# Kernel tuning notes

Measured on AMD Instinct MI355X. Metric: run time of the kernel, lower is better.

The kernel has to match this reference:

```python
import jax, jax.numpy as jnp
import numpy as np

B, T, D, H = 1, 2049, 1024, 16
HD = D // H                      # head_dim = 64
MAX_SEQ = 1025
L = 2 * MAX_SEQ - 1              # = T (required by the module's relative shift)

def setup_inputs() -> dict:
    key = jax.random.key(0)
    ks = jax.random.split(key, 12)
    s = 0.02
    return {
        'q': jax.random.normal(ks[0], (B, T, D), dtype=jnp.float32),
        'k': jax.random.normal(ks[1], (B, T, D), dtype=jnp.float32),
        'v': jax.random.normal(ks[2], (B, T, D), dtype=jnp.float32),
        'mask': jnp.tril(jnp.ones((1, 1, T, T), dtype=jnp.int32)),  # causal
        'Wq_w': jax.random.normal(ks[3], (D, D), dtype=jnp.float32) * s,
        'Wq_b': jnp.zeros((D,), dtype=jnp.float32),
        'Wk_w': jax.random.normal(ks[4], (D, D), dtype=jnp.float32) * s,
        'Wk_b': jnp.zeros((D,), dtype=jnp.float32),
        'Wv_w': jax.random.normal(ks[5], (D, D), dtype=jnp.float32) * s,
        'Wv_b': jnp.zeros((D,), dtype=jnp.float32),
        'Er': jax.random.normal(ks[6], (L, HD), dtype=jnp.float32),
        'Wo_w': jax.random.normal(ks[7], (D, D), dtype=jnp.float32) * s,
        'Wo_b': jnp.zeros((D,), dtype=jnp.float32),
    }

def reference(q, k, v, mask, Wq_w, Wq_b, Wk_w, Wk_b, Wv_w, Wv_b, Er, Wo_w, Wo_b):
    b, t, d = q.shape
    def proj(x, w, bias):
        # nn.Linear: x @ W^T + b ; then (B,T,H,HD) -> (B,H,T,HD)
        return (x @ w.T + bias).reshape(b, t, H, HD).transpose(0, 2, 1, 3)
    qh = proj(q, Wq_w, Wq_b)
    kh = proj(k, Wk_w, Wk_b)
    vh = proj(v, Wv_w, Wv_b)
    scores = jnp.einsum('bhtd,bhsd->bhts', qh, kh)          # (B,H,T,T)
    QEr = jnp.einsum('bhtd,ld->bhtl', qh, Er)               # (B,H,T,L) with L == T
    # _relative_shift: pad a zero row on seq dim then drop first row ->
    # row i becomes QEr row i+1, last row zeros (faithful to torch code)
    rel = jnp.concatenate([QEr[:, :, 1:, :], jnp.zeros_like(QEr[:, :, :1, :])], axis=2)
    scores = scores + rel
    scores = jnp.where(mask[:, :, :t, :t] == 0, -jnp.inf, scores)
    attn = jax.nn.softmax(scores / (HD ** 0.5), axis=-1)
    ctx = jnp.einsum('bhts,bhsd->bthd', attn, vh).reshape(b, t, d)
    return ctx @ Wo_w.T + Wo_b
```

## Files before the change

kernel.cpp:

```cpp
#include <hip/hip_runtime.h>
#include <hip/hip_bf16.h>
#include <math.h>

constexpr int T_SEQ = 2049;
constexpr int D_MODEL = 1024;
constexpr int N_HEAD = 16;
constexpr int HEAD_DIM = 64;
constexpr int VT_STRIDE = 2112;
constexpr int T1_ROWS = 1152;

typedef __attribute__((ext_vector_type(8))) short short8;
typedef __attribute__((ext_vector_type(4))) short short4v;
typedef __attribute__((ext_vector_type(4))) float floatx4;

__device__ inline void load_lds16(const void* g, void* l) {
  __builtin_amdgcn_global_load_lds(
      (const __attribute__((address_space(1))) unsigned int*)g,
      (__attribute__((address_space(3))) unsigned int*)l, 16, 0, 0);
}

__device__ inline short8 cvt8_bf16(const float* p) {
  float4 a = *(const float4*)p, b = *(const float4*)(p + 4);
  __hip_bfloat16 t[8] = {__float2bfloat16(a.x), __float2bfloat16(a.y),
                         __float2bfloat16(a.z), __float2bfloat16(a.w),
                         __float2bfloat16(b.x), __float2bfloat16(b.y),
                         __float2bfloat16(b.z), __float2bfloat16(b.w)};
  return *(const short8*)t;
}

__device__ inline float bf2f(__hip_bfloat16 x) { return __bfloat162float(x); }

__global__ __launch_bounds__(256) void cast_all(
    const float* __restrict__ q, const float* __restrict__ k,
    const float* __restrict__ v, const float* __restrict__ wq,
    const float* __restrict__ wk, const float* __restrict__ wv,
    const float* __restrict__ er, __hip_bfloat16* __restrict__ qo,
    __hip_bfloat16* __restrict__ ko, __hip_bfloat16* __restrict__ vo,
    __hip_bfloat16* __restrict__ wqo, __hip_bfloat16* __restrict__ wko,
    __hip_bfloat16* __restrict__ wvo, __hip_bfloat16* __restrict__ ero) {
  const int z = blockIdx.y;
  const float* in;
  __hip_bfloat16* out;
  int n;
  switch (z) {
    case 0: in = q; out = qo; n = T_SEQ * D_MODEL; break;
    case 1: in = k; out = ko; n = T_SEQ * D_MODEL; break;
    case 2: in = v; out = vo; n = T_SEQ * D_MODEL; break;
    case 3: in = wq; out = wqo; n = D_MODEL * D_MODEL; break;
    case 4: in = wk; out = wko; n = D_MODEL * D_MODEL; break;
    case 5: in = wv; out = wvo; n = D_MODEL * D_MODEL; break;
    default: in = er; out = ero; n = T_SEQ * HEAD_DIM; break;
  }
  const int i = (blockIdx.x * 256 + threadIdx.x) * 8;
  if (i + 8 > n) return;
  *(short8*)(out + i) = cvt8_bf16(in + i);
}

template <int BN, int OUTK>
__global__ __launch_bounds__(256) void mfma_gemm(
    const __hip_bfloat16* __restrict__ A0, const __hip_bfloat16* __restrict__ A1,
    const __hip_bfloat16* __restrict__ A2, const __hip_bfloat16* __restrict__ W0,
    const __hip_bfloat16* __restrict__ W1, const __hip_bfloat16* __restrict__ W2,
    const float* __restrict__ bias0, const float* __restrict__ bias1,
    const float* __restrict__ bias2, void* C0, void* C1, void* C2, int M) {
  constexpr int K = D_MODEL;
  constexpr int BK = 32;
  constexpr int NT = BN / 32;
  constexpr int AINST = 2;
  constexpr int BINST = BN / 64;
  constexpr int NLOADS = AINST + BINST;
  __shared__ __align__(16) char smem[128 * 64 * 2 + BN * 64 * 2];
  __hip_bfloat16* As = (__hip_bfloat16*)smem;
  __hip_bfloat16* Bs = (__hip_bfloat16*)(smem + 128 * 64 * 2);

  const int z = blockIdx.z;
  const short* A = (const short*)(z == 0 ? A0 : z == 1 ? A1 : A2);
  const short* W = (const short*)(z == 0 ? W0 : z == 1 ? W1 : W2);
  const float* bias = z == 0 ? bias0 : z == 1 ? bias1 : bias2;
  void* C = z == 0 ? C0 : z == 1 ? C1 : C2;

  const int tid = threadIdx.x;
  const int wave = tid >> 6, lane = tid & 63;
  const int col = lane & 15, quad = lane >> 4;
  const int wm = wave >> 1, wn = wave & 1;
  const int m0 = blockIdx.y * 128, n0 = blockIdx.x * BN;

  const int srow = lane >> 2;
  const int sslot = lane & 3;

  floatx4 acc[4][NT];
#pragma unroll
  for (int i = 0; i < 4; i++)
#pragma unroll
    for (int j = 0; j < NT; j++) acc[i][j] = (floatx4){0.f, 0.f, 0.f, 0.f};

#define STAGE_G(K0, BUF)                                                      \
  {                                                                           \
    _Pragma("unroll") for (int i = 0; i < AINST; i++) {                       \
      const int r_ = (wave * AINST + i) * 16 + srow;                          \
      const int ch = sslot ^ ((r_ >> 1) & 3);                                 \
      const int am = min(m0 + r_, M - 1);                                     \
      load_lds16(A + (size_t)am * K + (K0) + ch * 8,                          \
                 (char*)As + (BUF)*8192 + (wave * AINST + i) * 1024);         \
    }                                                                         \
    _Pragma("unroll") for (int i = 0; i < BINST; i++) {                       \
      const int r_ = (wave * BINST + i) * 16 + srow;                          \
      const int ch = sslot ^ ((r_ >> 1) & 3);                                 \
      load_lds16(W + (size_t)(n0 + r_) * K + (K0) + ch * 8,                   \
                 (char*)Bs + (BUF) * (BN * 64) + (wave * BINST + i) * 1024);  \
    }                                                                         \
  }

  STAGE_G(0, 0)

  int buf = 0;
  for (int k0 = 0; k0 < K; k0 += BK, buf ^= 1) {
    if (k0 + BK < K) {
      STAGE_G(k0 + BK, buf ^ 1)
      asm volatile("s_waitcnt vmcnt(%0)" ::"i"(NLOADS) : "memory");
    } else {
      asm volatile("s_waitcnt vmcnt(0)" ::: "memory");
    }
    __builtin_amdgcn_s_barrier();

    const __hip_bfloat16* as = As + buf * 4096;
    const __hip_bfloat16* bs = Bs + buf * (BN * 32);
    short8 af[4], bfr[NT];
#pragma unroll
    for (int t = 0; t < 4; t++) {
      const int ra = wm * 64 + t * 16 + col;
      af[t] = *(const short8*)(as + ra * 32 + ((quad ^ ((ra >> 1) & 3)) * 8));
    }
#pragma unroll
    for (int t = 0; t < NT; t++) {
      const int rb = wn * (BN / 2) + t * 16 + col;
      bfr[t] = *(const short8*)(bs + rb * 32 + ((quad ^ ((rb >> 1) & 3)) * 8));
    }
#pragma unroll
    for (int mt = 0; mt < 4; mt++)
#pragma unroll
      for (int nt = 0; nt < NT; nt++)
        acc[mt][nt] = __builtin_amdgcn_mfma_f32_16x16x32_bf16(af[mt], bfr[nt],
                                                              acc[mt][nt], 0, 0, 0);
    asm volatile("" ::: "memory");
    __builtin_amdgcn_s_barrier();
  }
#undef STAGE_G

  if (OUTK == 2 && z == 2) {
    short* Tt = (short*)smem;
#pragma unroll
    for (int mt = 0; mt < 4; mt++) {
      const int mb = wm * 16 + mt * 4 + quad;
#pragma unroll
      for (int nt = 0; nt < NT; nt++) {
        const int n = wn * (BN / 2) + nt * 16 + col;
        const float bb = bias[n0 + n];
        __hip_bfloat16 pk[4];
#pragma unroll
        for (int r = 0; r < 4; r++) pk[r] = __float2bfloat16(acc[mt][nt][r] + bb);
        *(short4v*)((char*)Tt + n * 256 + ((mb ^ (n & 15)) << 3)) =
            *(const short4v*)pk;
      }
    }
    __syncthreads();
    const int n_loc = tid >> 1, half = tid & 1;
    if (m0 + half * 64 < VT_STRIDE) {
      const int ng = n0 + n_loc;
      __hip_bfloat16* dst = (__hip_bfloat16*)C +
                            ((size_t)(ng >> 6) * HEAD_DIM + (ng & 63)) * VT_STRIDE +
                            m0 + half * 64;
#pragma unroll
      for (int c = 0; c < 8; c++) {
        short4v lo = *(const short4v*)((char*)Tt + n_loc * 256 +
                                       (((half * 16 + 2 * c) ^ (n_loc & 15)) << 3));
        short4v hi = *(const short4v*)((char*)Tt + n_loc * 256 +
                                       (((half * 16 + 2 * c + 1) ^ (n_loc & 15)) << 3));
        short8 o8 = {lo[0], lo[1], lo[2], lo[3], hi[0], hi[1], hi[2], hi[3]};
        *(short8*)((short*)dst + c * 8) = o8;
      }
    }
    return;
  }

#pragma unroll
  for (int mt = 0; mt < 4; mt++) {
#pragma unroll
    for (int r = 0; r < 4; r++) {
      const int m = m0 + wm * 64 + mt * 16 + quad * 4 + r;
      if (m >= M) continue;
#pragma unroll
      for (int nt = 0; nt < NT; nt++) {
        const int n = n0 + wn * (BN / 2) + nt * 16 + col;
        const float val = acc[mt][nt][r] + bias[n];
        if (OUTK == 0) {
          ((float*)C)[(size_t)m * D_MODEL + n] = val;
        } else {
          const int h = n >> 6, hd = n & 63;
          ((__hip_bfloat16*)C)[((size_t)h * T_SEQ + m) * HEAD_DIM + hd] =
              __float2bfloat16(val);
        }
      }
    }
  }
}

__global__ __launch_bounds__(512, 4) void flash_attn(
    const __hip_bfloat16* __restrict__ qh, const __hip_bfloat16* __restrict__ kh,
    const __hip_bfloat16* __restrict__ er, const __hip_bfloat16* __restrict__ vt,
    __hip_bfloat16* __restrict__ ctx, __hip_bfloat16* __restrict__ O0,
    __hip_bfloat16* __restrict__ O1, float* __restrict__ l0g,
    float* __restrict__ l1g) {
  __shared__ __align__(16) __hip_bfloat16 Ks[2][64 * 128];
  __shared__ __align__(16) __hip_bfloat16 Vs[2][64 * 64];
  __shared__ __align__(16) __hip_bfloat16 Ps[8][1024];

  const int tid = threadIdx.x;
  const int id = blockIdx.x + 26 * blockIdx.y;
  const int slot = id >> 3;
  const int h = (id & 7) + 8 * (slot >= 26);
  const int b = 25 - (slot >= 26 ? slot - 26 : slot);

  const int qt = (b < 8) ? b : 8 + ((b - 8) >> 1);
  const int tq0 = qt * 128;
  const int jmax = min(tq0 + 127, T_SEQ - 1) >> 6;
  int j0, j1;
  bool alt;
  if (b < 8) {
    j0 = 0; j1 = jmax; alt = false;
  } else {
    const int mid = (jmax + 1) >> 1;
    alt = (b - 8) & 1;
    j0 = alt ? mid : 0;
    j1 = alt ? jmax : mid - 1;
  }

  const int wave = tid >> 6;
  const int lane = tid & 63;
  const int col = lane & 15;
  const int quad = lane >> 4;

  const short* qplane = (const short*)(qh + (size_t)h * T_SEQ * HEAD_DIM);
  const short* kplane = (const short*)(kh + (size_t)h * T_SEQ * HEAD_DIM);
  const short* eplane = (const short*)er;
  const short* vplane = (const short*)(vt + (size_t)h * HEAD_DIM * VT_STRIDE);

  const int t_abs = tq0 + wave * 16 + col;
  const int tload = min(t_abs, T_SEQ - 1);
  const bool hiz = (t_abs >= T_SEQ - 1);
  short8 aq[4];
#pragma unroll
  for (int kc = 0; kc < 4; kc++) {
    short8 v = *(const short8*)(qplane + (size_t)tload * 64 + kc * 32 + quad * 8);
    if (kc >= 2 && hiz) v = (short8){0, 0, 0, 0, 0, 0, 0, 0};
    aq[kc] = v;
  }

  floatx4 o[4];
  float l_lane = 0.f;
#pragma unroll
  for (int i = 0; i < 4; i++) o[i] = (floatx4){0.f, 0.f, 0.f, 0.f};

  const int tstrip = tq0 + wave * 16;
  __hip_bfloat16* psw = &Ps[wave][0];

#define STAGE_TILE(JJ, BUF)                                                        \
  {                                                                                \
    const int s0_ = (JJ) * 64;                                                     \
    _Pragma("unroll") for (int ii = 0; ii < 2; ii++) {                             \
      const int i_ = wave * 2 + ii;                                                \
      const int r_ = i_ * 4 + (lane >> 4);                                         \
      const int sl_ = lane & 15;                                                   \
      const int g_ = (sl_ & 8) | ((sl_ ^ (r_ & 7)) & 7);                           \
      const int s_ = min(s0_ + r_, T_SEQ - 1);                                     \
      const short* src_ = (g_ < 8) ? (kplane + (size_t)s_ * 64 + g_ * 8)           \
                                   : (eplane + (size_t)s_ * 64 + (g_ - 8) * 8);    \
      load_lds16(src_, (char*)&Ks[BUF][0] + i_ * 1024);                            \
    }                                                                              \
    {                                                                              \
      const int d_ = wave * 8 + (lane >> 3);                                       \
      const int sl_ = lane & 7;                                                    \
      const int g_ = sl_ ^ (d_ & 7);                                               \
      load_lds16(vplane + (size_t)d_ * VT_STRIDE + s0_ + g_ * 8,                   \
                 (char*)&Vs[BUF][0] + wave * 1024);                                \
    }                                                                              \
  }

  STAGE_TILE(j0, 0)
  int buf = 0;

  for (int j = j0; j <= j1; ++j, buf ^= 1) {
    __syncthreads();
    if (j < j1) STAGE_TILE(j + 1, buf ^ 1)

    const int s0 = j * 64;
    if (s0 > tstrip + 15) continue;

    const __hip_bfloat16* ks = &Ks[buf][0];
    const __hip_bfloat16* vs = &Vs[buf][0];

    floatx4 sacc[4];
    __builtin_amdgcn_s_setprio(1);
#pragma unroll
    for (int st = 0; st < 4; st++) {
      floatx4 c = {0.f, 0.f, 0.f, 0.f};
      const int row = st * 16 + col;
#pragma unroll
      for (int kc = 0; kc < 4; kc++) {
        const int ch = kc * 4 + quad;
        const int slot2 = (ch & 8) | ((ch ^ (row & 7)) & 7);
        short8 ka = *(const short8*)(ks + row * 128 + slot2 * 8);
        c = __builtin_amdgcn_mfma_f32_16x16x32_bf16(ka, aq[kc], c, 0, 0, 0);
      }
      sacc[st] = c;
    }
    __builtin_amdgcn_s_setprio(0);

    if (s0 + 63 > tstrip) {
#pragma unroll
      for (int st = 0; st < 4; st++) {
        const int sbase = s0 + st * 16 + quad * 4;
#pragma unroll
        for (int r = 0; r < 4; r++)
          if (sbase + r > t_abs) sacc[st][r] = -INFINITY;
      }
    }

    float rs = 0.f;
#pragma unroll
    for (int st = 0; st < 4; st++)
#pragma unroll
      for (int r = 0; r < 4; r++) {
        const float p = __expf(sacc[st][r] * 0.125f);
        sacc[st][r] = p;
        rs += p;
      }
    l_lane += rs;

#pragma unroll
    for (int st = 0; st < 4; st++) {
      __hip_bfloat16 pb[4];
#pragma unroll
      for (int r = 0; r < 4; r++) pb[r] = __float2bfloat16(sacc[st][r]);
      const int kcA = st >> 1;
      const int quadA = (st & 1) * 2 + (quad >> 1);
      const int off = ((kcA * 4 + quadA) * 16 + col) * 8 + (quad & 1) * 4;
      *(short4v*)(psw + off) = *(const short4v*)pb;
    }
    short8 pa[2];
#pragma unroll
    for (int kc = 0; kc < 2; kc++)
      pa[kc] = *(const short8*)(psw + ((kc * 4 + quad) * 16 + col) * 8);

    __builtin_amdgcn_s_setprio(1);
#pragma unroll
    for (int nt = 0; nt < 4; nt++) {
      const int row = nt * 16 + col;
#pragma unroll
      for (int kc = 0; kc < 2; kc++) {
        const int slot2 = (kc * 4 + quad) ^ (row & 7);
        short8 vb = *(const short8*)(vs + row * 64 + slot2 * 8);
        o[nt] = __builtin_amdgcn_mfma_f32_16x16x32_bf16(pa[kc], vb, o[nt], 0, 0, 0);
      }
    }
    __builtin_amdgcn_s_setprio(0);
  }

  l_lane += __shfl_xor(l_lane, 16, 64);
  l_lane += __shfl_xor(l_lane, 32, 64);

  if (b < 8) {
    const float linv = 1.0f / l_lane;
    float linv_r[4];
#pragma unroll
    for (int r = 0; r < 4; r++) linv_r[r] = __shfl(linv, quad * 4 + r, 64);
#pragma unroll
    for (int r = 0; r < 4; r++) {
      const int t = tstrip + quad * 4 + r;
#pragma unroll
      for (int nt = 0; nt < 4; nt++)
        ctx[(size_t)t * D_MODEL + h * 64 + nt * 16 + col] =
            __float2bfloat16(o[nt][r] * linv_r[r]);
    }
  } else {
    if (lane < 16) {
      const int t = tstrip + lane;
      if (t < T_SEQ) {
        if (!alt)
          l0g[h * T1_ROWS + (t - 1024)] = l_lane;
        else
          l1g[h * T1_ROWS + (t - 1024)] = l_lane;
      }
    }
#pragma unroll
    for (int r = 0; r < 4; r++) {
      const int t = tstrip + quad * 4 + r;
      if (t < T_SEQ) {
        __hip_bfloat16* dst = (!alt ? O0 : O1) + (size_t)(t - 1024) * D_MODEL;
#pragma unroll
        for (int nt = 0; nt < 4; nt++)
          dst[h * 64 + nt * 16 + col] = __float2bfloat16(o[nt][r]);
      }
    }
  }
}

__global__ __launch_bounds__(256) void finalize(
    const __hip_bfloat16* __restrict__ O0, const __hip_bfloat16* __restrict__ O1,
    const float* __restrict__ l0g, const float* __restrict__ l1g,
    __hip_bfloat16* __restrict__ ctx, const float* __restrict__ wo_src,
    __hip_bfloat16* __restrict__ wob) {
  if (blockIdx.y == 1) {
    const int i = (blockIdx.x * 256 + threadIdx.x) * 8;
    if (i + 8 <= D_MODEL * D_MODEL) *(short8*)(wob + i) = cvt8_bf16(wo_src + i);
    return;
  }
  const int idx = blockIdx.x * 256 + threadIdx.x;
  const int tr = idx >> 7;
  const int t = 1024 + tr;
  if (t >= T_SEQ) return;
  const int ch = idx & 127;
  const int h = ch >> 3;

  const float l = l0g[h * T1_ROWS + tr] + l1g[h * T1_ROWS + tr];
  const __hip_bfloat16* a = O0 + (size_t)tr * D_MODEL + ch * 8;
  const __hip_bfloat16* bsrc = O1 + (size_t)tr * D_MODEL + ch * 8;
  const float inv = 1.0f / l;
  __hip_bfloat16 outv[8];
#pragma unroll
  for (int i = 0; i < 8; i++)
    outv[i] = __float2bfloat16((bf2f(a[i]) + bf2f(bsrc[i])) * inv);
  *(short8*)(ctx + (size_t)t * D_MODEL + ch * 8) = *(const short8*)outv;
}

extern "C" void kernel_launch(void* const* d_in, const int* in_sizes, int n_in,
                              void* d_out, int out_size, void* d_ws, size_t ws_size,
                              hipStream_t stream) {
  const float* q = (const float*)d_in[0];
  const float* k = (const float*)d_in[1];
  const float* v = (const float*)d_in[2];
  const float* Wq_w = (const float*)d_in[4];
  const float* Wq_b = (const float*)d_in[5];
  const float* Wk_w = (const float*)d_in[6];
  const float* Wk_b = (const float*)d_in[7];
  const float* Wv_w = (const float*)d_in[8];
  const float* Wv_b = (const float*)d_in[9];
  const float* Er = (const float*)d_in[10];
  const float* Wo_w = (const float*)d_in[11];
  const float* Wo_b = (const float*)d_in[12];
  float* out = (float*)d_out;

  char* ws = (char*)d_ws;
  const size_t sz_plane = (size_t)T_SEQ * D_MODEL * 2;
  const size_t sz_w = (size_t)D_MODEL * D_MODEL * 2;
  const size_t sz_vt = (size_t)N_HEAD * HEAD_DIM * VT_STRIDE * 2;
  const size_t sz_er = (size_t)T_SEQ * HEAD_DIM * 2;
  const size_t sz_Op = (size_t)T1_ROWS * D_MODEL * 2;
  const size_t sz_l = (size_t)N_HEAD * T1_ROWS * 4;

  __hip_bfloat16* qbf = (__hip_bfloat16*)ws;
  __hip_bfloat16* kbf = (__hip_bfloat16*)(ws + sz_plane);
  __hip_bfloat16* vbf = (__hip_bfloat16*)(ws + 2 * sz_plane);
  __hip_bfloat16* wqb = (__hip_bfloat16*)(ws + 3 * sz_plane);
  __hip_bfloat16* wkb = (__hip_bfloat16*)(ws + 3 * sz_plane + sz_w);
  __hip_bfloat16* wvb = (__hip_bfloat16*)(ws + 3 * sz_plane + 2 * sz_w);
  char* hi = ws + 3 * sz_plane + 3 * sz_w;
  __hip_bfloat16* qpr = (__hip_bfloat16*)hi;
  __hip_bfloat16* kpr = (__hip_bfloat16*)(hi + sz_plane);
  __hip_bfloat16* vt = (__hip_bfloat16*)(hi + 2 * sz_plane);
  __hip_bfloat16* er_bf = (__hip_bfloat16*)(hi + 2 * sz_plane + sz_vt);

  __hip_bfloat16* ctxb = (__hip_bfloat16*)ws;
  __hip_bfloat16* O0 = (__hip_bfloat16*)(ws + sz_plane);
  __hip_bfloat16* O1 = (__hip_bfloat16*)(ws + sz_plane + sz_Op);
  float* l0g = (float*)(ws + sz_plane + 2 * sz_Op);
  float* l1g = (float*)(ws + sz_plane + 2 * sz_Op + sz_l);
  __hip_bfloat16* wob = (__hip_bfloat16*)(ws + 3 * sz_plane);

  const dim3 blk(256);

  cast_all<<<dim3(1025, 7), blk, 0, stream>>>(q, k, v, Wq_w, Wk_w, Wv_w, Er, qbf,
                                              kbf, vbf, wqb, wkb, wvb, er_bf);

  mfma_gemm<128, 2><<<dim3(8, 17, 3), blk, 0, stream>>>(
      qbf, kbf, vbf, wqb, wkb, wvb, Wq_b, Wk_b, Wv_b, qpr, kpr, vt, T_SEQ);

  flash_attn<<<dim3(26, N_HEAD), dim3(512), 0, stream>>>(qpr, kpr, er_bf, vt, ctxb,
                                                         O0, O1, l0g, l1g);

  finalize<<<dim3((1025 * 128 + 255) / 256, 2), blk, 0, stream>>>(
      O0, O1, l0g, l1g, ctxb, Wo_w, wob);

  mfma_gemm<64, 0><<<dim3(16, 17, 1), blk, 0, stream>>>(
      ctxb, ctxb, ctxb, wob, wob, wob, Wo_b, Wo_b, Wo_b, out, out, out, T_SEQ);
}
```

Before: 192.6 us.

## Fuse fp32-to-bf16 casts into GEMM loaders and merge split-attention finalize into output GEMM

Removes the standalone cast kernel and the finalize kernel. The QKV GEMM now reads fp32 activations and weights directly, converts them to bf16 in registers and writes them into LDS through a software-pipelined register prefetch, and the Er cast rides along as an extra z-slice. The output GEMM merges the two partial attention outputs with their softmax normalizers inside its A-loader and converts Wo on the fly. This cuts two launches and the bf16 intermediate write/read traffic, but the GEMMs now load twice the bytes per element and lose the async global-to-LDS loads, and each weight tile is reconverted by every M-block.

New measurement: 208.3 us. 8.2% more time.

```diff
diff --git a/kernel.cpp b/kernel.cpp
--- a/kernel.cpp
+++ b/kernel.cpp
@@ -28,133 +28,133 @@
   return *(const short8*)t;
 }
 
+__device__ inline short8 cvt8_pair(float4 a, float4 b) {
+  __hip_bfloat16 t[8] = {__float2bfloat16(a.x), __float2bfloat16(a.y),
+                         __float2bfloat16(a.z), __float2bfloat16(a.w),
+                         __float2bfloat16(b.x), __float2bfloat16(b.y),
+                         __float2bfloat16(b.z), __float2bfloat16(b.w)};
+  return *(const short8*)t;
+}
+
 __device__ inline float bf2f(__hip_bfloat16 x) { return __bfloat162float(x); }
 
-__global__ __launch_bounds__(256) void cast_all(
+__global__ __launch_bounds__(256) void qkv_gemm(
     const float* __restrict__ q, const float* __restrict__ k,
     const float* __restrict__ v, const float* __restrict__ wq,
     const float* __restrict__ wk, const float* __restrict__ wv,
-    const float* __restrict__ er, __hip_bfloat16* __restrict__ qo,
-    __hip_bfloat16* __restrict__ ko, __hip_bfloat16* __restrict__ vo,
-    __hip_bfloat16* __restrict__ wqo, __hip_bfloat16* __restrict__ wko,
-    __hip_bfloat16* __restrict__ wvo, __hip_bfloat16* __restrict__ ero) {
-  const int z = blockIdx.y;
-  const float* in;
-  __hip_bfloat16* out;
-  int n;
-  switch (z) {
-    case 0: in = q; out = qo; n = T_SEQ * D_MODEL; break;
-    case 1: in = k; out = ko; n = T_SEQ * D_MODEL; break;
-    case 2: in = v; out = vo; n = T_SEQ * D_MODEL; break;
-    case 3: in = wq; out = wqo; n = D_MODEL * D_MODEL; break;
-    case 4: in = wk; out = wko; n = D_MODEL * D_MODEL; break;
-    case 5: in = wv; out = wvo; n = D_MODEL * D_MODEL; break;
-    default: in = er; out = ero; n = T_SEQ * HEAD_DIM; break;
-  }
-  const int i = (blockIdx.x * 256 + threadIdx.x) * 8;
-  if (i + 8 > n) return;
-  *(short8*)(out + i) = cvt8_bf16(in + i);
-}
-
-template <int BN, int OUTK>
-__global__ __launch_bounds__(256) void mfma_gemm(
-    const __hip_bfloat16* __restrict__ A0, const __hip_bfloat16* __restrict__ A1,
-    const __hip_bfloat16* __restrict__ A2, const __hip_bfloat16* __restrict__ W0,
-    const __hip_bfloat16* __restrict__ W1, const __hip_bfloat16* __restrict__ W2,
-    const float* __restrict__ bias0, const float* __restrict__ bias1,
-    const float* __restrict__ bias2, void* C0, void* C1, void* C2, int M) {
-  constexpr int K = D_MODEL;
-  constexpr int BK = 32;
-  constexpr int NT = BN / 32;
-  constexpr int AINST = 2;
-  constexpr int BINST = BN / 64;
-  constexpr int NLOADS = AINST + BINST;
-  __shared__ __align__(16) char smem[128 * 64 * 2 + BN * 64 * 2];
-  __hip_bfloat16* As = (__hip_bfloat16*)smem;
-  __hip_bfloat16* Bs = (__hip_bfloat16*)(smem + 128 * 64 * 2);
-
+    const float* __restrict__ bq, const float* __restrict__ bk,
+    const float* __restrict__ bv, __hip_bfloat16* __restrict__ qpr,
+    __hip_bfloat16* __restrict__ kpr, __hip_bfloat16* __restrict__ vt,
+    const float* __restrict__ er, __hip_bfloat16* __restrict__ er_bf) {
   const int z = blockIdx.z;
-  const short* A = (const short*)(z == 0 ? A0 : z == 1 ? A1 : A2);
-  const short* W = (const short*)(z == 0 ? W0 : z == 1 ? W1 : W2);
-  const float* bias = z == 0 ? bias0 : z == 1 ? bias1 : bias2;
-  void* C = z == 0 ? C0 : z == 1 ? C1 : C2;
+  if (z == 3) {
+    const int id = blockIdx.x + 8 * blockIdx.y;
+    const int i = (id * 256 + threadIdx.x) * 8;
+    if (i + 8 <= T_SEQ * HEAD_DIM) *(short8*)(er_bf + i) = cvt8_bf16(er + i);
+    return;
+  }
+  constexpr int K = D_MODEL, BK = 32, NS = K / BK;
+  __shared__ __align__(16) char smem[32768];
+
+  const float* A = z == 0 ? q : z == 1 ? k : v;
+  const float* W = z == 0 ? wq : z == 1 ? wk : wv;
+  const float* bias = z == 0 ? bq : z == 1 ? bk : bv;
 
   const int tid = threadIdx.x;
   const int wave = tid >> 6, lane = tid & 63;
   const int col = lane & 15, quad = lane >> 4;
   const int wm = wave >> 1, wn = wave & 1;
-  const int m0 = blockIdx.y * 128, n0 = blockIdx.x * BN;
-
-  const int srow = lane >> 2;
-  const int sslot = lane & 3;
-
-  floatx4 acc[4][NT];
+  const int m0 = blockIdx.y * 128, n0 = blockIdx.x * 128;
+  const int srow = lane >> 2, sslot = lane & 3;
+
+  int rrow[2], rch[2], ram[2];
+#pragma unroll
+  for (int i = 0; i < 2; i++) {
+    rrow[i] = (wave * 2 + i) * 16 + srow;
+    rch[i] = sslot ^ ((rrow[i] >> 1) & 3);
+    ram[i] = min(m0 + rrow[i], T_SEQ - 1);
+  }
+
+  float4 ra[2][2], rb[2][2];
+  short8 SA[2], SB[2];
+
+#define LOADS(K0)                                                          \
+  {                                                                        \
+    _Pragma("unroll") for (int i = 0; i < 2; i++) {                        \
+      const float* p = A + (size_t)ram[i] * K + (K0) + rch[i] * 8;         \
+      ra[i][0] = *(const float4*)p;                                        \
+      ra[i][1] = *(const float4*)(p + 4);                                  \
+      const float* pw = W + (size_t)(n0 + rrow[i]) * K + (K0) + rch[i] * 8;\
+      rb[i][0] = *(const float4*)pw;                                       \
+      rb[i][1] = *(const float4*)(pw + 4);                                 \
+    }                                                                      \
+  }
+#define CVT()                                                              \
+  {                                                                        \
+    _Pragma("unroll") for (int i = 0; i < 2; i++) {                        \
+      SA[i] = cvt8_pair(ra[i][0], ra[i][1]);                               \
+      SB[i] = cvt8_pair(rb[i][0], rb[i][1]);                               \
+    }                                                                      \
+  }
+
+  floatx4 acc[4][4];
 #pragma unroll
   for (int i = 0; i < 4; i++)
 #pragma unroll
-    for (int j = 0; j < NT; j++) acc[i][j] = (floatx4){0.f, 0.f, 0.f, 0.f};
-
-#define STAGE_G(K0, BUF)                                                      \
-  {                                                                           \
-    _Pragma("unroll") for (int i = 0; i < AINST; i++) {                       \
-      const int r_ = (wave * AINST + i) * 16 + srow;                          \
-      const int ch = sslot ^ ((r_ >> 1) & 3);                                 \
-      const int am = min(m0 + r_, M - 1);                                     \
-      load_lds16(A + (size_t)am * K + (K0) + ch * 8,                          \
-                 (char*)As + (BUF)*8192 + (wave * AINST + i) * 1024);         \
-    }                                                                         \
-    _Pragma("unroll") for (int i = 0; i < BINST; i++) {                       \
-      const int r_ = (wave * BINST + i) * 16 + srow;                          \
-      const int ch = sslot ^ ((r_ >> 1) & 3);                                 \
-      load_lds16(W + (size_t)(n0 + r_) * K + (K0) + ch * 8,                   \
-                 (char*)Bs + (BUF) * (BN * 64) + (wave * BINST + i) * 1024);  \
-    }                                                                         \
-  }
-
-  STAGE_G(0, 0)
-
-  int buf = 0;
-  for (int k0 = 0; k0 < K; k0 += BK, buf ^= 1) {
-    if (k0 + BK < K) {
-      STAGE_G(k0 + BK, buf ^ 1)
-      asm volatile("s_waitcnt vmcnt(%0)" ::"i"(NLOADS) : "memory");
-    } else {
-      asm volatile("s_waitcnt vmcnt(0)" ::: "memory");
-    }
+    for (int j = 0; j < 4; j++) acc[i][j] = (floatx4){0.f, 0.f, 0.f, 0.f};
+
+  LOADS(0)
+  CVT()
+  LOADS(BK)
+
+  for (int s = 0; s < NS; ++s) {
+    const int buf = s & 1;
+#pragma unroll
+    for (int i = 0; i < 2; i++) {
+      *(short8*)(smem + buf * 8192 + rrow[i] * 64 + sslot * 16) = SA[i];
+      *(short8*)(smem + 16384 + buf * 8192 + rrow[i] * 64 + sslot * 16) = SB[i];
+    }
+    asm volatile("s_waitcnt lgkmcnt(0)" ::: "memory");
+    __builtin_amdgcn_sched_barrier(0);
     __builtin_amdgcn_s_barrier();
 
-    const __hip_bfloat16* as = As + buf * 4096;
-    const __hip_bfloat16* bs = Bs + buf * (BN * 32);
-    short8 af[4], bfr[NT];
+    const __hip_bfloat16* as = (const __hip_bfloat16*)(smem + buf * 8192);
+    const __hip_bfloat16* bs = (const __hip_bfloat16*)(smem + 16384 + buf * 8192);
+    short8 af[4], bfr[4];
 #pragma unroll
     for (int t = 0; t < 4; t++) {
-      const int ra = wm * 64 + t * 16 + col;
-      af[t] = *(const short8*)(as + ra * 32 + ((quad ^ ((ra >> 1) & 3)) * 8));
-    }
-#pragma unroll
-    for (int t = 0; t < NT; t++) {
-      const int rb = wn * (BN / 2) + t * 16 + col;
-      bfr[t] = *(const short8*)(bs + rb * 32 + ((quad ^ ((rb >> 1) & 3)) * 8));
+      const int ra_ = wm * 64 + t * 16 + col;
+      af[t] = *(const short8*)(as + ra_ * 32 + ((quad ^ ((ra_ >> 1) & 3)) * 8));
+    }
+#pragma unroll
+    for (int t = 0; t < 4; t++) {
+      const int rb_ = wn * 64 + t * 16 + col;
+      bfr[t] = *(const short8*)(bs + rb_ * 32 + ((quad ^ ((rb_ >> 1) & 3)) * 8));
     }
 #pragma unroll
     for (int mt = 0; mt < 4; mt++)
 #pragma unroll
-      for (int nt = 0; nt < NT; nt++)
+      for (int nt = 0; nt < 4; nt++)
         acc[mt][nt] = __builtin_amdgcn_mfma_f32_16x16x32_bf16(af[mt], bfr[nt],
                                                               acc[mt][nt], 0, 0, 0);
-    asm volatile("" ::: "memory");
-    __builtin_amdgcn_s_barrier();
-  }
-#undef STAGE_G
-
-  if (OUTK == 2 && z == 2) {
+    if (s + 1 < NS) {
+      __builtin_amdgcn_sched_barrier(0);
+      CVT()
+      if (s + 2 < NS) LOADS((s + 2) * BK)
+    }
+  }
+#undef LOADS
+#undef CVT
+
+  if (z == 2) {
+    __syncthreads();
     short* Tt = (short*)smem;
 #pragma unroll
     for (int mt = 0; mt < 4; mt++) {
       const int mb = wm * 16 + mt * 4 + quad;
 #pragma unroll
-      for (int nt = 0; nt < NT; nt++) {
-        const int n = wn * (BN / 2) + nt * 16 + col;
+      for (int nt = 0; nt < 4; nt++) {
+        const int n = wn * 64 + nt * 16 + col;
         const float bb = bias[n0 + n];
         __hip_bfloat16 pk[4];
 #pragma unroll
@@ -167,7 +167,7 @@
     const int n_loc = tid >> 1, half = tid & 1;
     if (m0 + half * 64 < VT_STRIDE) {
       const int ng = n0 + n_loc;
-      __hip_bfloat16* dst = (__hip_bfloat16*)C +
+      __hip_bfloat16* dst = vt +
                             ((size_t)(ng >> 6) * HEAD_DIM + (ng & 63)) * VT_STRIDE +
                             m0 + half * 64;
 #pragma unroll
@@ -183,23 +183,150 @@
     return;
   }
 
+  __hip_bfloat16* C = z == 0 ? qpr : kpr;
 #pragma unroll
   for (int mt = 0; mt < 4; mt++) {
 #pragma unroll
     for (int r = 0; r < 4; r++) {
       const int m = m0 + wm * 64 + mt * 16 + quad * 4 + r;
-      if (m >= M) continue;
-#pragma unroll
-      for (int nt = 0; nt < NT; nt++) {
-        const int n = n0 + wn * (BN / 2) + nt * 16 + col;
+      if (m >= T_SEQ) continue;
+#pragma unroll
+      for (int nt = 0; nt < 4; nt++) {
+        const int n = n0 + wn * 64 + nt * 16 + col;
         const float val = acc[mt][nt][r] + bias[n];
-        if (OUTK == 0) {
-          ((float*)C)[(size_t)m * D_MODEL + n] = val;
-        } else {
-          const int h = n >> 6, hd = n & 63;
-          ((__hip_bfloat16*)C)[((size_t)h * T_SEQ + m) * HEAD_DIM + hd] =
-              __float2bfloat16(val);
-        }
+        const int h = n >> 6, hd = n & 63;
+        C[((size_t)h * T_SEQ + m) * HEAD_DIM + hd] = __float2bfloat16(val);
+      }
+    }
+  }
+}
+
+__global__ __launch_bounds__(256) void out_gemm(
+    const __hip_bfloat16* __restrict__ ctxb, const __hip_bfloat16* __restrict__ O0,
+    const __hip_bfloat16* __restrict__ O1, const float* __restrict__ l0g,
+    const float* __restrict__ l1g, const float* __restrict__ wo,
+    const float* __restrict__ bias, float* __restrict__ out) {
+  constexpr int K = D_MODEL, BK = 32, NS = K / BK, BN = 64;
+  __shared__ __align__(16) char smem[24576];
+
+  const int tid = threadIdx.x;
+  const int wave = tid >> 6, lane = tid & 63;
+  const int col = lane & 15, quad = lane >> 4;
+  const int wm = wave >> 1, wn = wave & 1;
+  const int m0 = blockIdx.y * 128, n0 = blockIdx.x * BN;
+  const int srow = lane >> 2, sslot = lane & 3;
+  const bool merge = (m0 >= 1024);
+
+  int rrow[2], rch[2], ram[2];
+#pragma unroll
+  for (int i = 0; i < 2; i++) {
+    rrow[i] = (wave * 2 + i) * 16 + srow;
+    rch[i] = sslot ^ ((rrow[i] >> 1) & 3);
+    ram[i] = min(m0 + rrow[i], T_SEQ - 1);
+  }
+  const int brow = wave * 16 + srow;
+  const int bch = sslot ^ ((brow >> 1) & 3);
+
+  short8 SA[2], SB;
+  float4 rb[2];
+  short8 raw0[2], raw1[2];
+  float lsum[2];
+
+#define LOADS(K0)                                                            \
+  {                                                                          \
+    _Pragma("unroll") for (int i = 0; i < 2; i++) {                          \
+      const int kb = (K0) + rch[i] * 8;                                      \
+      if (!merge) {                                                          \
+        raw0[i] = *(const short8*)(ctxb + (size_t)ram[i] * K + kb);          \
+      } else {                                                               \
+        const int tr = ram[i] - 1024;                                        \
+        const int hk = kb >> 6;                                              \
+        raw0[i] = *(const short8*)(O0 + (size_t)tr * K + kb);                \
+        raw1[i] = *(const short8*)(O1 + (size_t)tr * K + kb);                \
+        lsum[i] = l0g[hk * T1_ROWS + tr] + l1g[hk * T1_ROWS + tr];           \
+      }                                                                      \
+    }                                                                        \
+    const float* pw = wo + (size_t)(n0 + brow) * K + (K0) + bch * 8;         \
+    rb[0] = *(const float4*)pw;                                              \
+    rb[1] = *(const float4*)(pw + 4);                                        \
+  }
+#define CVT()                                                                \
+  {                                                                          \
+    _Pragma("unroll") for (int i = 0; i < 2; i++) {                          \
+      if (!merge) {                                                          \
+        SA[i] = raw0[i];                                                     \
+      } else {                                                               \
+        const float inv = 1.0f / lsum[i];                                    \
+        __hip_bfloat16 t[8];                                                 \
+        _Pragma("unroll") for (int e = 0; e < 8; e++) {                      \
+          t[e] = __float2bfloat16(                                           \
+              (bf2f(((const __hip_bfloat16*)&raw0[i])[e]) +                  \
+               bf2f(((const __hip_bfloat16*)&raw1[i])[e])) * inv);           \
+        }                                                                    \
+        SA[i] = *(const short8*)t;                                           \
+      }                                                                      \
+    }                                                                        \
+    SB = cvt8_pair(rb[0], rb[1]);                                            \
+  }
+
+  floatx4 acc[4][2];
+#pragma unroll
+  for (int i = 0; i < 4; i++)
+#pragma unroll
+    for (int j = 0; j < 2; j++) acc[i][j] = (floatx4){0.f, 0.f, 0.f, 0.f};
+
+  LOADS(0)
+  CVT()
+  LOADS(BK)
+
+  for (int s = 0; s < NS; ++s) {
+    const int buf = s & 1;
+#pragma unroll
+    for (int i = 0; i < 2; i++)
+      *(short8*)(smem + buf * 8192 + rrow[i] * 64 + sslot * 16) = SA[i];
+    *(short8*)(smem + 16384 + buf * 4096 + brow * 64 + sslot * 16) = SB;
+    asm volatile("s_waitcnt lgkmcnt(0)" ::: "memory");
+    __builtin_amdgcn_sched_barrier(0);
+    __builtin_amdgcn_s_barrier();
+
+    const __hip_bfloat16* as = (const __hip_bfloat16*)(smem + buf * 8192);
+    const __hip_bfloat16* bs = (const __hip_bfloat16*)(smem + 16384 + buf * 4096);
+    short8 af[4], bfr[2];
+#pragma unroll
+    for (int t = 0; t < 4; t++) {
+      const int ra_ = wm * 64 + t * 16 + col;
+      af[t] = *(const short8*)(as + ra_ * 32 + ((quad ^ ((ra_ >> 1) & 3)) * 8));
+    }
+#pragma unroll
+    for (int t = 0; t < 2; t++) {
+      const int rb_ = wn * 32 + t * 16 + col;
+      bfr[t] = *(const short8*)(bs + rb_ * 32 + ((quad ^ ((rb_ >> 1) & 3)) * 8));
+    }
+#pragma unroll
+    for (int mt = 0; mt < 4; mt++)
+#pragma unroll
+      for (int nt = 0; nt < 2; nt++)
+        acc[mt][nt] = __builtin_amdgcn_mfma_f32_16x16x32_bf16(af[mt], bfr[nt],
+                                                              acc[mt][nt], 0, 0, 0);
+    if (s + 1 < NS) {
+      __builtin_amdgcn_sched_barrier(0);
+      CVT()
+      if (s + 2 < NS) LOADS((s + 2) * BK)
+    }
+  }
+#undef LOADS
+#undef CVT
+
+#pragma unroll
+  for (int mt = 0; mt < 4; mt++) {
+#pragma unroll
+    for (int r = 0; r < 4; r++) {
+      const int m = m0 + wm * 64 + mt * 16 + quad * 4 + r;
+      if (m >= T_SEQ) continue;
+#pragma unroll
+      for (int nt = 0; nt < 2; nt++) {
+        const int n = n0 + wn * 32 + nt * 16 + col;
+        out[(size_t)m * D_MODEL + n] = acc[mt][nt][r] + bias[n];
       }
     }
   }
@@ -405,34 +532,6 @@
   }
 }
 
-__global__ __launch_bounds__(256) void finalize(
-    const __hip_bfloat16* __restrict__ O0, const __hip_bfloat16* __restrict__ O1,
-    const float* __restrict__ l0g, const float* __restrict__ l1g,
-    __hip_bfloat16* __restrict__ ctx, const float* __restrict__ wo_src,
-    __hip_bfloat16* __restrict__ wob) {
-  if (blockIdx.y == 1) {
-    const int i = (blockIdx.x * 256 + threadIdx.x) * 8;
-    if (i + 8 <= D_MODEL * D_MODEL) *(short8*)(wob + i) = cvt8_bf16(wo_src + i);
-    return;
-  }
-  const int idx = blockIdx.x * 256 + threadIdx.x;
-  const int tr = idx >> 7;
-  const int t = 1024 + tr;
-  if (t >= T_SEQ) return;
-  const int ch = idx & 127;
-  const int h = ch >> 3;
-
-  const float l = l0g[h * T1_ROWS + tr] + l1g[h * T1_ROWS + tr];
-  const __hip_bfloat16* a = O0 + (size_t)tr * D_MODEL + ch * 8;
-  const __hip_bfloat16* bsrc = O1 + (size_t)tr * D_MODEL + ch * 8;
-  const float inv = 1.0f / l;
-  __hip_bfloat16 outv[8];
-#pragma unroll
-  for (int i = 0; i < 8; i++)
-    outv[i] = __float2bfloat16((bf2f(a[i]) + bf2f(bsrc[i])) * inv);
-  *(short8*)(ctx + (size_t)t * D_MODEL + ch * 8) = *(const short8*)outv;
-}
-
 extern "C" void kernel_launch(void* const* d_in, const int* in_sizes, int n_in,
                               void* d_out, int out_size, void* d_ws, size_t ws_size,
                               hipStream_t stream) {
@@ -452,45 +551,29 @@
 
   char* ws = (char*)d_ws;
   const size_t sz_plane = (size_t)T_SEQ * D_MODEL * 2;
-  const size_t sz_w = (size_t)D_MODEL * D_MODEL * 2;
   const size_t sz_vt = (size_t)N_HEAD * HEAD_DIM * VT_STRIDE * 2;
   const size_t sz_er = (size_t)T_SEQ * HEAD_DIM * 2;
+  const size_t sz_ctx = (size_t)1024 * D_MODEL * 2;
   const size_t sz_Op = (size_t)T1_ROWS * D_MODEL * 2;
   const size_t sz_l = (size_t)N_HEAD * T1_ROWS * 4;
 
-  __hip_bfloat16* qbf = (__hip_bfloat16*)ws;
-  __hip_bfloat16* kbf = (__hip_bfloat16*)(ws + sz_plane);
-  __hip_bfloat16* vbf = (__hip_bfloat16*)(ws + 2 * sz_plane);
-  __hip_bfloat16* wqb = (__hip_bfloat16*)(ws + 3 * sz_plane);
-  __hip_bfloat16* wkb = (__hip_bfloat16*)(ws + 3 * sz_plane + sz_w);
-  __hip_bfloat16* wvb = (__hip_bfloat16*)(ws + 3 * sz_plane + 2 * sz_w);
-  char* hi = ws + 3 * sz_plane + 3 * sz_w;
-  __hip_bfloat16* qpr = (__hip_bfloat16*)hi;
-  __hip_bfloat16* kpr = (__hip_bfloat16*)(hi + sz_plane);
-  __hip_bfloat16* vt = (__hip_bfloat16*)(hi + 2 * sz_plane);
-  __hip_bfloat16* er_bf = (__hip_bfloat16*)(hi + 2 * sz_plane + sz_vt);
-
-  __hip_bfloat16* ctxb = (__hip_bfloat16*)ws;
-  __hip_bfloat16* O0 = (__hip_bfloat16*)(ws + sz_plane);
-  __hip_bfloat16* O1 = (__hip_bfloat16*)(ws + sz_plane + sz_Op);
-  float* l0g = (float*)(ws + sz_plane + 2 * sz_Op);
-  float* l1g = (float*)(ws + sz_plane + 2 * sz_Op + sz_l);
-  __hip_bfloat16* wob = (__hip_bfloat16*)(ws + 3 * sz_plane);
-
-  const dim3 blk(256);
-
-  cast_all<<<dim3(1025, 7), blk, 0, stream>>>(q, k, v, Wq_w, Wk_w, Wv_w, Er, qbf,
-                                              kbf, vbf, wqb, wkb, wvb, er_bf);
-
-  mfma_gemm<128, 2><<<dim3(8, 17, 3), blk, 0, stream>>>(
-      qbf, kbf, vbf, wqb, wkb, wvb, Wq_b, Wk_b, Wv_b, qpr, kpr, vt, T_SEQ);
+  __hip_bfloat16* qpr = (__hip_bfloat16*)ws;
+  __hip_bfloat16* kpr = (__hip_bfloat16*)(ws + sz_plane);
+  __hip_bfloat16* vt = (__hip_bfloat16*)(ws + 2 * sz_plane);
+  __hip_bfloat16* er_bf = (__hip_bfloat16*)(ws + 2 * sz_plane + sz_vt);
+  __hip_bfloat16* ctxb = (__hip_bfloat16*)(ws + 2 * sz_plane + sz_vt + sz_er);
+  char* ob = ws + 2 * sz_plane + sz_vt + sz_er + sz_ctx;
+  __hip_bfloat16* O0 = (__hip_bfloat16*)ob;
+  __hip_bfloat16* O1 = (__hip_bfloat16*)(ob + sz_Op);
+  float* l0g = (float*)(ob + 2 * sz_Op);
+  float* l1g = (float*)(ob + 2 * sz_Op + sz_l);
+
+  qkv_gemm<<<dim3(8, 17, 4), dim3(256), 0, stream>>>(
+      q, k, v, Wq_w, Wk_w, Wv_w, Wq_b, Wk_b, Wv_b, qpr, kpr, vt, Er, er_bf);
 
   flash_attn<<<dim3(26, N_HEAD), dim3(512), 0, stream>>>(qpr, kpr, er_bf, vt, ctxb,
                                                          O0, O1, l0g, l1g);
 
-  finalize<<<dim3((1025 * 128 + 255) / 256, 2), blk, 0, stream>>>(
-      O0, O1, l0g, l1g, ctxb, Wo_w, wob);
-
-  mfma_gemm<64, 0><<<dim3(16, 17, 1), blk, 0, stream>>>(
-      ctxb, ctxb, ctxb, wob, wob, wob, Wo_b, Wo_b, Wo_b, out, out, out, T_SEQ);
-}
+  out_gemm<<<dim3(16, 17), dim3(256), 0, stream>>>(ctxb, O0, O1, l0g, l1g, Wo_w,
+                                                   Wo_b, out);
+}
```
